# Kernel optimization log

Hardware: AMD Instinct MI355X
Metric: run time of the kernel (lower is better)

## Reference

```python
import jax, jax.numpy as jnp
import numpy as np

N = 50000      # total nodes across batch of graphs
E = 800000     # total directed edges (avg degree 16)
B = 64         # number of graphs
D = 128        # input_dim == hidden_dim
L = 4          # num_layers - 1 GIN layers
OUT = 10
BN_EPS = 1e-5


def setup_inputs() -> dict:
    key = jax.random.key(0)
    ks = jax.random.split(key, 12)
    s = 0.05
    return {
        "x": jax.random.normal(ks[0], (N, D), jnp.float32),
        "pi": jax.random.uniform(ks[1], (B, 25), jnp.float32),
        "eps": jnp.zeros((L,), jnp.float32),
        "mlp_w1": jax.random.normal(ks[2], (L, D, D), jnp.float32) * s,
        "mlp_b1": jnp.zeros((L, D), jnp.float32),
        "mlp_bn_g": jnp.ones((L, D), jnp.float32),
        "mlp_bn_b": jnp.zeros((L, D), jnp.float32),
        "mlp_w2": jax.random.normal(ks[3], (L, D, D), jnp.float32) * s,
        "mlp_b2": jnp.zeros((L, D), jnp.float32),
        "bn_g": jnp.ones((L, D), jnp.float32),
        "bn_b": jnp.zeros((L, D), jnp.float32),
        "attend_w": jax.random.normal(ks[4], (D * (L + 1), 1), jnp.float32) * s,
        "attend_b": jnp.zeros((1,), jnp.float32),
        "pi_w": jax.random.normal(ks[5], (25, 16), jnp.float32) * s,
        "pi_b": jnp.zeros((16,), jnp.float32),
        "out_w": jax.random.normal(ks[6], (D * (L + 1) + 16, OUT), jnp.float32) * s,
        "out_b": jnp.zeros((OUT,), jnp.float32),
        "edge_index": jax.random.randint(ks[7], (2, E), 0, N, dtype=jnp.int32),
        "graph_id": jnp.sort(jax.random.randint(ks[8], (N,), 0, B, dtype=jnp.int32)),
    }


def _bn(z, g, b):
    # BatchNorm1d in training mode over all nodes (axis 0)
    m = z.mean(axis=0)
    v = z.var(axis=0)
    return (z - m) * jax.lax.rsqrt(v + BN_EPS) * g + b


def reference(x, pi, eps, mlp_w1, mlp_b1, mlp_bn_g, mlp_bn_b, mlp_w2, mlp_b2,
              bn_g, bn_b, attend_w, attend_b, pi_w, pi_b, out_w, out_b,
              edge_index, graph_id):
    src, dst = edge_index[0], edge_index[1]
    h = x
    reps = [x]
    for l in range(L):
        # GIN sum aggregation (learn_eps=True: no self-loops in Adj)
        pooled = jax.ops.segment_sum(h[src], dst, num_segments=N)
        pooled = pooled + (1.0 + eps[l]) * h
        # 2-layer MLP: Linear -> BN -> ReLU -> Linear
        z = jax.nn.relu(_bn(pooled @ mlp_w1[l] + mlp_b1[l], mlp_bn_g[l], mlp_bn_b[l]))
        z = z @ mlp_w2[l] + mlp_b2[l]
        # outer BN + ReLU
        h = jax.nn.relu(_bn(z, bn_g[l], bn_b[l]))
        reps.append(h)
    hr = jnp.concatenate(reps, axis=1)               # [N, D*(L+1)]
    # per-graph attention softmax over nodes
    scores = (hr @ attend_w + attend_b)[:, 0]        # [N]
    smax = jax.ops.segment_max(scores, graph_id, num_segments=B)
    e = jnp.exp(scores - smax[graph_id])
    denom = jax.ops.segment_sum(e, graph_id, num_segments=B)
    coef = e / denom[graph_id]
    gemb = jax.ops.segment_sum(hr * coef[:, None], graph_id, num_segments=B)  # [B, D*(L+1)]
    # persistence-image branch (PI computed host-side; treated as input)
    pie = jax.nn.relu(pi @ pi_w + pi_b)              # [B, 16]
    feat = jnp.concatenate([gemb, pie], axis=1)      # [B, D*(L+1)+16]
    return feat @ out_w + out_b                      # [B, OUT]
```

## Files before the change

### kernel.cpp

```cpp
#include <hip/hip_runtime.h>
#include <hip/hip_bf16.h>

#define NN 50000
#define EE 800000
#define BBG 64
#define DD 128
#define LLAY 4
#define HRW 640
#define NOUT 10
#define SCANB 196
#define NXCD 8

typedef __hip_bfloat16 bf16;
typedef __attribute__((ext_vector_type(8))) short short8;
typedef __attribute__((ext_vector_type(4))) float f32x4;

__device__ __forceinline__ float b2f(bf16 v) { return __bfloat162float(v); }
__device__ __forceinline__ float bflo(unsigned u) { return __uint_as_float(u << 16); }
__device__ __forceinline__ float bfhi(unsigned u) { return __uint_as_float(u & 0xffff0000u); }
__device__ __forceinline__ unsigned short f2bs(float v) {
  bf16 h = __float2bfloat16(v);
  unsigned short r; __builtin_memcpy(&r, &h, 2); return r;
}
__device__ __forceinline__ int dtype_of(const void* __restrict__ bng) {
  return (*(const unsigned*)bng == 0x3F800000u) ? 1 : 0;
}
__device__ __forceinline__ float ldf(const void* __restrict__ p, long i, int dt) {
  return dt ? ((const float*)p)[i] : b2f(((const bf16*)p)[i]);
}

__device__ __forceinline__ int xccid() {
  unsigned v;
  asm("s_getreg_b32 %0, hwreg(HW_REG_XCC_ID)" : "=s"(v));
  return (int)(v & (NXCD - 1));
}

__device__ __forceinline__ void fadd_l2(float* p, float v) {
  asm volatile("global_atomic_add_f32 %0, %1, off" :: "v"(p), "v"(v) : "memory");
}

__device__ __forceinline__ int lower_bound_i(const int* __restrict__ a, int n, int key) {
  int lo = 0, hi = n;
  while (lo < hi) { int mid = (lo + hi) >> 1; if (a[mid] < key) lo = mid + 1; else hi = mid; }
  return lo;
}

__global__ __launch_bounds__(256) void gnn_init(const void* __restrict__ x,
                                                bf16* __restrict__ hrb,
                                                const void* __restrict__ w1,
                                                const void* __restrict__ w2,
                                                bf16* __restrict__ w1t,
                                                bf16* __restrict__ w2t,
                                                const void* __restrict__ aw,
                                                float* __restrict__ scores,
                                                const int* __restrict__ ei,
                                                int* __restrict__ cnt,
                                                int* __restrict__ rel,
                                                const void* __restrict__ bng) {
  int dt = dtype_of(bng);
  int tid = threadIdx.x;
  if (blockIdx.x >= 6250) {
    int i = (blockIdx.x - 6250) * 256 + tid;
    int l = i >> 14, rem = i & 16383, n = rem >> 7, k = rem & 127;
    long src = (long)l * 16384 + k * 128 + n;
    w1t[i] = __float2bfloat16(ldf(w1, src, dt));
    w2t[i] = __float2bfloat16(ldf(w2, src, dt));
    return;
  }
  if (blockIdx.x >= 3125) {
    int e = (blockIdx.x - 3125) * 256 + tid;
    int dst = ei[EE + e];
    int xid = xccid();
    int old = __hip_atomic_fetch_add(&cnt[(size_t)xid * NN + dst], 1,
                                     __ATOMIC_RELAXED, __HIP_MEMORY_SCOPE_WORKGROUP);
    rel[e] = (xid << 24) | old;
    return;
  }
  int n = blockIdx.x * 16 + (tid >> 4);
  int il = tid & 15;
  long base = (long)n * DD + il * 8;
  float v[8];
  if (dt) {
    float4 a0 = *(const float4*)((const float*)x + base);
    float4 a1 = *(const float4*)((const float*)x + base + 4);
    v[0] = a0.x; v[1] = a0.y; v[2] = a0.z; v[3] = a0.w;
    v[4] = a1.x; v[5] = a1.y; v[6] = a1.z; v[7] = a1.w;
  } else {
    uint4 u = *(const uint4*)((const bf16*)x + base);
    v[0] = bflo(u.x); v[1] = bfhi(u.x); v[2] = bflo(u.y); v[3] = bfhi(u.y);
    v[4] = bflo(u.z); v[5] = bfhi(u.z); v[6] = bflo(u.w); v[7] = bfhi(u.w);
  }
  uint4 o;
  o.x = (unsigned)f2bs(v[0]) | ((unsigned)f2bs(v[1]) << 16);
  o.y = (unsigned)f2bs(v[2]) | ((unsigned)f2bs(v[3]) << 16);
  o.z = (unsigned)f2bs(v[4]) | ((unsigned)f2bs(v[5]) << 16);
  o.w = (unsigned)f2bs(v[6]) | ((unsigned)f2bs(v[7]) << 16);
  *(uint4*)(hrb + (size_t)n * HRW + il * 8) = o;
  float ss = 0.f;
  #pragma unroll
  for (int k = 0; k < 8; k++) ss += v[k] * ldf(aw, il * 8 + k, dt);
  ss += __shfl_xor(ss, 1, 64); ss += __shfl_xor(ss, 2, 64);
  ss += __shfl_xor(ss, 4, 64); ss += __shfl_xor(ss, 8, 64);
  if (il == 0) scores[n] = ss;
}

__global__ __launch_bounds__(256) void gnn_scan1(const int* __restrict__ cnt,
                                                 int* __restrict__ blocksum) {
  __shared__ int buf[256];
  int tid = threadIdx.x;
  int i = blockIdx.x * 256 + tid;
  int v = 0;
  if (i < NN) {
    #pragma unroll
    for (int k = 0; k < NXCD; k++) v += cnt[(size_t)k * NN + i];
  }
  buf[tid] = v;
  __syncthreads();
  for (int s = 128; s > 0; s >>= 1) {
    if (tid < s) buf[tid] += buf[tid + s];
    __syncthreads();
  }
  if (tid == 0) blocksum[blockIdx.x] = buf[0];
}

__global__ __launch_bounds__(256) void gnn_scan3(int* __restrict__ cnt,
                                                 const int* __restrict__ blocksum,
                                                 int* __restrict__ rowstart) {
  __shared__ int buf[256];
  int tid = threadIdx.x;
  int partial = 0;
  for (int i = tid; i < blockIdx.x; i += 256) partial += blocksum[i];
  buf[tid] = partial;
  __syncthreads();
  for (int s = 128; s > 0; s >>= 1) {
    if (tid < s) buf[tid] += buf[tid + s];
    __syncthreads();
  }
  int offset = buf[0];
  __syncthreads();
  int i = blockIdx.x * 256 + tid;
  int c[NXCD];
  int v = 0;
  if (i < NN) {
    #pragma unroll
    for (int k = 0; k < NXCD; k++) { c[k] = cnt[(size_t)k * NN + i]; v += c[k]; }
  }
  buf[tid] = v;
  __syncthreads();
  for (int ofs = 1; ofs < 256; ofs <<= 1) {
    int t = (tid >= ofs) ? buf[tid - ofs] : 0;
    __syncthreads();
    buf[tid] += t;
    __syncthreads();
  }
  int val = offset + buf[tid] - v;
  if (i < NN) {
    rowstart[i] = val;
    int run = val;
    #pragma unroll
    for (int k = 0; k < NXCD; k++) { cnt[(size_t)k * NN + i] = run; run += c[k]; }
  }
  if (blockIdx.x == SCANB - 1 && tid == 255) rowstart[NN] = offset + buf[255];
}

__global__ __launch_bounds__(256) void gnn_fill(const int* __restrict__ ei,
                                                const int* __restrict__ xcdpre,
                                                const int* __restrict__ rel,
                                                int* __restrict__ csr_src) {
  int e = blockIdx.x * 256 + threadIdx.x;
  int src = ei[e];
  int dst = ei[EE + e];
  int r = rel[e];
  int xid = r >> 24;
  int rank = r & 0xFFFFFF;
  csr_src[xcdpre[(size_t)xid * NN + dst] + rank] = src;
}

__device__ __forceinline__ void acc8(float* a, uint4 u) {
  a[0] += bflo(u.x); a[1] += bfhi(u.x);
  a[2] += bflo(u.y); a[3] += bfhi(u.y);
  a[4] += bflo(u.z); a[5] += bfhi(u.z);
  a[6] += bflo(u.w); a[7] += bfhi(u.w);
}

__device__ __forceinline__ float2 statsum(const float* __restrict__ stat, int c) {
  float s = 0.f, q = 0.f;
  #pragma unroll
  for (int k = 0; k < 8; k++) { s += stat[k * 256 + c]; q += stat[k * 256 + 128 + c]; }
  return make_float2(s, q);
}

__global__ __launch_bounds__(512) void gnn_gmg1(const bf16* __restrict__ hrb, int l,
                                                const int* __restrict__ rowstart,
                                                const int* __restrict__ csr_src,
                                                const void* __restrict__ eps,
                                                const bf16* __restrict__ Wt,
                                                const void* __restrict__ bias, int biasOfs,
                                                bf16* __restrict__ out,
                                                float* __restrict__ statOut,
                                                const void* __restrict__ bng) {
  int dt = dtype_of(bng);
  __shared__ __align__(16) unsigned ar[16][68];
  __shared__ int qhead;
  int tid = threadIdx.x, lane = tid & 63;
  int w = tid >> 6;
  int q = lane >> 4, il = lane & 15;
  int r0 = blockIdx.x * 16;
  const bf16* stripe = hrb + l * DD;
  float s = 1.0f + ldf(eps, l, dt);
  if (tid == 0) qhead = 0;
  __syncthreads();

  for (;;) {
    int i;
    if (lane == 0) i = atomicAdd(&qhead, 1);
    i = __shfl(i, 0, 64);
    if (i >= 16) break;
    int n = r0 + i;
    float a[8] = {0.f, 0.f, 0.f, 0.f, 0.f, 0.f, 0.f, 0.f};
    if (q == 0) {
      uint4 u = *(const uint4*)(stripe + (size_t)n * HRW + il * 8);
      a[0] = s * bflo(u.x); a[1] = s * bfhi(u.x);
      a[2] = s * bflo(u.y); a[3] = s * bfhi(u.y);
      a[4] = s * bflo(u.z); a[5] = s * bfhi(u.z);
      a[6] = s * bflo(u.w); a[7] = s * bfhi(u.w);
    }
    int start = rowstart[n], end = rowstart[n + 1];
    for (int base = start; base < end; base += 64) {
      int m = end - base; if (m > 64) m = 64;
      int idx = (base + lane < end) ? csr_src[base + lane] : 0;
      int j = 0;
      for (; j + 16 <= m; j += 16) {
        int s0 = __shfl(idx, j + q, 64);
        int s1 = __shfl(idx, j + 4 + q, 64);
        int s2 = __shfl(idx, j + 8 + q, 64);
        int s3 = __shfl(idx, j + 12 + q, 64);
        uint4 u0 = *(const uint4*)(stripe + (size_t)s0 * HRW + il * 8);
        uint4 u1 = *(const uint4*)(stripe + (size_t)s1 * HRW + il * 8);
        uint4 u2 = *(const uint4*)(stripe + (size_t)s2 * HRW + il * 8);
        uint4 u3 = *(const uint4*)(stripe + (size_t)s3 * HRW + il * 8);
        acc8(a, u0); acc8(a, u1); acc8(a, u2); acc8(a, u3);
      }
      for (; j + 8 <= m; j += 8) {
        int s0 = __shfl(idx, j + q, 64);
        int s1 = __shfl(idx, j + 4 + q, 64);
        uint4 u0 = *(const uint4*)(stripe + (size_t)s0 * HRW + il * 8);
        uint4 u1 = *(const uint4*)(stripe + (size_t)s1 * HRW + il * 8);
        acc8(a, u0); acc8(a, u1);
      }
      for (; j + 4 <= m; j += 4) {
        int src = __shfl(idx, j + q, 64);
        uint4 u = *(const uint4*)(stripe + (size_t)src * HRW + il * 8);
        acc8(a, u);
      }
      for (; j < m; j++) {
        int src = __shfl(idx, j, 64);
        if (q == 0) {
          uint4 u = *(const uint4*)(stripe + (size_t)src * HRW + il * 8);
          acc8(a, u);
        }
      }
    }
    #pragma unroll
    for (int k = 0; k < 8; k++) {
      a[k] += __shfl_xor(a[k], 16, 64);
      a[k] += __shfl_xor(a[k], 32, 64);
    }
    if (q == 0) {
      uint4 o;
      o.x = (unsigned)f2bs(a[0]) | ((unsigned)f2bs(a[1]) << 16);
      o.y = (unsigned)f2bs(a[2]) | ((unsigned)f2bs(a[3]) << 16);
      o.z = (unsigned)f2bs(a[4]) | ((unsigned)f2bs(a[5]) << 16);
      o.w = (unsigned)f2bs(a[6]) | ((unsigned)f2bs(a[7]) << 16);
      *(uint4*)&ar[i][il * 4] = o;
    }
  }
  __syncthreads();

  f32x4 acc = (f32x4){0.f, 0.f, 0.f, 0.f};
  #pragma unroll
  for (int ch = 0; ch < 4; ch++) {
    int k0 = ch * 32 + q * 8;
    uint4 raw = *(const uint4*)&ar[il][ch * 16 + q * 4];
    short8 af;
    __builtin_memcpy(&af, &raw, 16);
    short8 bfv = *(const short8*)(Wt + (w * 16 + il) * DD + k0);
    acc = __builtin_amdgcn_mfma_f32_16x16x32_bf16(af, bfv, acc, 0, 0, 0);
  }
  int col = w * 16 + il;
  float bv = ldf(bias, biasOfs + col, dt);
  float ss = 0.f, qq = 0.f;
  #pragma unroll
  for (int r = 0; r < 4; r++) {
    int row = r0 + q * 4 + r;
    float v = acc[r] + bv;
    out[(size_t)row * DD + col] = __float2bfloat16(v);
    ss += v; qq += v * v;
  }
  ss += __shfl_xor(ss, 16, 64);  ss += __shfl_xor(ss, 32, 64);
  qq += __shfl_xor(qq, 16, 64);  qq += __shfl_xor(qq, 32, 64);
  if (q == 0) {
    int xid = xccid();
    fadd_l2(&statOut[xid * 256 + col], ss);
    fadd_l2(&statOut[xid * 256 + 128 + col], qq);
  }
}

__global__ __launch_bounds__(256) void gnn_mgemm(const bf16* __restrict__ Abf,
                                                 const bf16* __restrict__ Wt,
                                                 const void* __restrict__ bias, int biasOfs,
                                                 bf16* __restrict__ out,
                                                 const float* __restrict__ statIn,
                                                 const void* __restrict__ g,
                                                 const void* __restrict__ bb, int parOfs,
                                                 float* __restrict__ statOut,
                                                 const void* __restrict__ bng) {
  int dt = dtype_of(bng);
  __shared__ float scf[128], shf[128];
  __shared__ float redS[4][128], redQ[4][128];
  int tid = threadIdx.x, w = tid >> 6, lane = tid & 63;
  int q = lane >> 4, il = lane & 15;
  if (tid < 128) {
    const float invN = 1.0f / NN;
    float2 sq = statsum(statIn, tid);
    float m = sq.x * invN;
    float rs = rsqrtf(sq.y * invN - m * m + 1e-5f);
    float gg = ldf(g, parOfs + tid, dt), bv = ldf(bb, parOfs + tid, dt);
    scf[tid] = rs * gg;
    shf[tid] = bv - m * rs * gg;
  }
  __syncthreads();
  int r0 = (blockIdx.x * 4 + w) * 16;
  int arow = r0 + il;
  int arowc = (arow < NN) ? arow : (NN - 1);
  f32x4 acc[8];
  #pragma unroll
  for (int i = 0; i < 8; i++) acc[i] = (f32x4){0.f, 0.f, 0.f, 0.f};
  #pragma unroll
  for (int ch = 0; ch < 4; ch++) {
    int k0 = ch * 32 + q * 8;
    uint4 raw = *(const uint4*)(Abf + (size_t)arowc * DD + k0);
    float4 c0 = *(const float4*)(scf + k0);
    float4 c1 = *(const float4*)(scf + k0 + 4);
    float4 d0 = *(const float4*)(shf + k0);
    float4 d1 = *(const float4*)(shf + k0 + 4);
    short8 af;
    af[0] = (short)f2bs(fmaxf(bflo(raw.x) * c0.x + d0.x, 0.f));
    af[1] = (short)f2bs(fmaxf(bfhi(raw.x) * c0.y + d0.y, 0.f));
    af[2] = (short)f2bs(fmaxf(bflo(raw.y) * c0.z + d0.z, 0.f));
    af[3] = (short)f2bs(fmaxf(bfhi(raw.y) * c0.w + d0.w, 0.f));
    af[4] = (short)f2bs(fmaxf(bflo(raw.z) * c1.x + d1.x, 0.f));
    af[5] = (short)f2bs(fmaxf(bfhi(raw.z) * c1.y + d1.y, 0.f));
    af[6] = (short)f2bs(fmaxf(bflo(raw.w) * c1.z + d1.z, 0.f));
    af[7] = (short)f2bs(fmaxf(bfhi(raw.w) * c1.w + d1.w, 0.f));
    #pragma unroll
    for (int ct = 0; ct < 8; ct++) {
      short8 bfv = *(const short8*)(Wt + (ct * 16 + il) * DD + k0);
      acc[ct] = __builtin_amdgcn_mfma_f32_16x16x32_bf16(af, bfv, acc[ct], 0, 0, 0);
    }
  }
  #pragma unroll
  for (int ct = 0; ct < 8; ct++) {
    int col = ct * 16 + il;
    float bv = ldf(bias, biasOfs + col, dt);
    float s = 0.f, qq = 0.f;
    #pragma unroll
    for (int r = 0; r < 4; r++) {
      int row = r0 + q * 4 + r;
      float v = acc[ct][r] + bv;
      if (row < NN) {
        out[(size_t)row * DD + col] = __float2bfloat16(v);
        s += v; qq += v * v;
      }
    }
    s += __shfl_xor(s, 16, 64);  s += __shfl_xor(s, 32, 64);
    qq += __shfl_xor(qq, 16, 64); qq += __shfl_xor(qq, 32, 64);
    if (q == 0) { redS[w][col] = s; redQ[w][col] = qq; }
  }
  __syncthreads();
  int xid = xccid();
  if (tid < 128) {
    float v = redS[0][tid] + redS[1][tid] + redS[2][tid] + redS[3][tid];
    fadd_l2(&statOut[xid * 256 + tid], v);
  } else {
    int c = tid - 128;
    float v = redQ[0][c] + redQ[1][c] + redQ[2][c] + redQ[3][c];
    fadd_l2(&statOut[xid * 256 + 128 + c], v);
  }
}

__global__ __launch_bounds__(256) void gnn_bn_relu(const bf16* __restrict__ z2,
                                                   const float* __restrict__ stat,
                                                   const void* __restrict__ g,
                                                   const void* __restrict__ bb, int parOfs,
                                                   bf16* __restrict__ hrb, int stripe,
                                                   const void* __restrict__ aw,
                                                   float* __restrict__ scores,
                                                   const void* __restrict__ bng) {
  int dt = dtype_of(bng);
  __shared__ float scf[128], shf[128], awf[128];
  int tid = threadIdx.x;
  if (tid < 128) {
    const float invN = 1.0f / NN;
    float2 sq = statsum(stat, tid);
    float m = sq.x * invN;
    float rs = rsqrtf(sq.y * invN - m * m + 1e-5f);
    float gg = ldf(g, parOfs + tid, dt), bv = ldf(bb, parOfs + tid, dt);
    scf[tid] = rs * gg;
    shf[tid] = bv - m * rs * gg;
    awf[tid] = ldf(aw, stripe * DD + tid, dt);
  }
  __syncthreads();
  int n = blockIdx.x * 16 + (tid >> 4);
  int il = tid & 15;
  int c0 = il * 8;
  uint4 u = *(const uint4*)(z2 + (size_t)n * DD + c0);
  float v[8];
  v[0] = bflo(u.x); v[1] = bfhi(u.x); v[2] = bflo(u.y); v[3] = bfhi(u.y);
  v[4] = bflo(u.z); v[5] = bfhi(u.z); v[6] = bflo(u.w); v[7] = bfhi(u.w);
  float ss = 0.f;
  #pragma unroll
  for (int k = 0; k < 8; k++) {
    v[k] = fmaxf(v[k] * scf[c0 + k] + shf[c0 + k], 0.f);
    ss += v[k] * awf[c0 + k];
  }
  uint4 o;
  o.x = (unsigned)f2bs(v[0]) | ((unsigned)f2bs(v[1]) << 16);
  o.y = (unsigned)f2bs(v[2]) | ((unsigned)f2bs(v[3]) << 16);
  o.z = (unsigned)f2bs(v[4]) | ((unsigned)f2bs(v[5]) << 16);
  o.w = (unsigned)f2bs(v[6]) | ((unsigned)f2bs(v[7]) << 16);
  *(uint4*)(hrb + (size_t)n * HRW + stripe * DD + c0) = o;
  ss += __shfl_xor(ss, 1, 64); ss += __shfl_xor(ss, 2, 64);
  ss += __shfl_xor(ss, 4, 64); ss += __shfl_xor(ss, 8, 64);
  if (il == 0) scores[n] += ss;
}

__global__ __launch_bounds__(128) void gnn_gemb(const bf16* __restrict__ hrb,
                                                const float* __restrict__ scores,
                                                const int* __restrict__ gid,
                                                float* __restrict__ gemb) {
  int b = blockIdx.x / 40;
  int part = blockIdx.x % 40;
  int chunk = part % 5;
  int slice = part / 5;
  int tid = threadIdx.x;
  int start = lower_bound_i(gid, NN, b);
  int end = lower_bound_i(gid, NN, b + 1);
  __shared__ float red[128];
  float mx = -3.4e38f;
  for (int n = start + tid; n < end; n += 128) mx = fmaxf(mx, scores[n]);
  red[tid] = mx;
  __syncthreads();
  for (int s = 64; s > 0; s >>= 1) {
    if (tid < s) red[tid] = fmaxf(red[tid], red[tid + s]);
    __syncthreads();
  }
  float smax = red[0];
  __syncthreads();
  float sum = 0.f;
  for (int n = start + tid; n < end; n += 128) sum += __expf(scores[n] - smax);
  red[tid] = sum;
  __syncthreads();
  for (int s = 64; s > 0; s >>= 1) {
    if (tid < s) red[tid] += red[tid + s];
    __syncthreads();
  }
  float denom = red[0];
  float inv = (denom > 0.f) ? 1.0f / denom : 0.f;
  int c = chunk * 128 + tid;
  float acc = 0.f;
  for (int n = start + slice; n < end; n += 8)
    acc += b2f(hrb[(size_t)n * HRW + c]) * __expf(scores[n] - smax) * inv;
  unsafeAtomicAdd(&gemb[b * HRW + c], acc);
}

__global__ __launch_bounds__(64) void gnn_final(const float* __restrict__ gemb,
                                                const void* __restrict__ pi,
                                                const void* __restrict__ piw,
                                                const void* __restrict__ pib,
                                                const void* __restrict__ ow,
                                                const void* __restrict__ ob,
                                                void* __restrict__ out,
                                                const void* __restrict__ bng) {
  int dt = dtype_of(bng);
  int b = blockIdx.x;
  int t = threadIdx.x;
  __shared__ float pie[16];
  if (t < 16) {
    float s = ldf(pib, t, dt);
    for (int i = 0; i < 25; i++) s += ldf(pi, b * 25 + i, dt) * ldf(piw, i * 16 + t, dt);
    pie[t] = fmaxf(s, 0.f);
  }
  __syncthreads();
  for (int o = 0; o < NOUT; o++) {
    float s = 0.f;
    for (int c = t; c < HRW + 16; c += 64) {
      float f = (c < HRW) ? gemb[b * HRW + c] : pie[c - HRW];
      s += f * ldf(ow, c * NOUT + o, dt);
    }
    #pragma unroll
    for (int m = 32; m > 0; m >>= 1) s += __shfl_xor(s, m, 64);
    if (t == 0) {
      float r = s + ldf(ob, o, dt);
      if (dt) ((float*)out)[b * NOUT + o] = r;
      else ((bf16*)out)[b * NOUT + o] = __float2bfloat16(r);
    }
  }
}

extern "C" void kernel_launch(void* const* d_in, const int* in_sizes, int n_in,
                              void* d_out, int out_size, void* d_ws, size_t ws_size,
                              hipStream_t stream) {
  const void* x    = d_in[0];
  const void* pi   = d_in[1];
  const void* eps  = d_in[2];
  const void* w1   = d_in[3];
  const void* b1   = d_in[4];
  const void* bng  = d_in[5];
  const void* bnb  = d_in[6];
  const void* w2   = d_in[7];
  const void* b2   = d_in[8];
  const void* obng = d_in[9];
  const void* obnb = d_in[10];
  const void* aw   = d_in[11];
  const void* piw  = d_in[13];
  const void* pib  = d_in[14];
  const void* ow   = d_in[15];
  const void* ob   = d_in[16];
  const int*  ei   = (const int*)d_in[17];
  const int*  gid  = (const int*)d_in[18];

  bf16*  hrb      = (bf16*)d_ws;
  bf16*  z1       = hrb + (size_t)NN * HRW;
  bf16*  z2       = z1 + (size_t)NN * DD;
  bf16*  w1t      = z2 + (size_t)NN * DD;
  bf16*  w2t      = w1t + LLAY * DD * DD;
  float* statbufs = (float*)(w2t + LLAY * DD * DD);
  float* gemb     = statbufs + 8 * 2048;
  int*   cnt      = (int*)(gemb + BBG * HRW);
  size_t zeroBytes = (size_t)(8 * 2048 + BBG * HRW + NXCD * NN) * 4;
  float* scores   = (float*)(cnt + (size_t)NXCD * NN);
  int*   rowstart = (int*)(scores + NN);
  int*   rel      = rowstart + NN + 1;
  int*   csr_src  = rel + EE;
  int*   blocksum = csr_src + EE;

  hipMemsetAsync(statbufs, 0, zeroBytes, stream);
  gnn_init<<<6506, 256, 0, stream>>>(x, hrb, w1, w2, w1t, w2t, aw, scores,
                                     ei, cnt, rel, bng);

  gnn_scan1<<<SCANB, 256, 0, stream>>>(cnt, blocksum);
  gnn_scan3<<<SCANB, 256, 0, stream>>>(cnt, blocksum, rowstart);
  gnn_fill<<<EE / 256, 256, 0, stream>>>(ei, cnt, rel, csr_src);

  for (int l = 0; l < LLAY; l++) {
    float* statA = statbufs + (l * 2 + 0) * 2048;
    float* statB = statbufs + (l * 2 + 1) * 2048;
    gnn_gmg1<<<NN / 16, 512, 0, stream>>>(hrb, l, rowstart, csr_src, eps,
                                          w1t + l * DD * DD, b1, l * DD,
                                          z1, statA, bng);
    gnn_mgemm<<<782, 256, 0, stream>>>(z1, w2t + l * DD * DD, b2, l * DD,
                                       z2, statA, bng, bnb, l * DD,
                                       statB, bng);
    gnn_bn_relu<<<NN / 16, 256, 0, stream>>>(z2, statB, obng, obnb, l * DD,
                                             hrb, l + 1, aw, scores, bng);
  }

  gnn_gemb<<<BBG * 40, 128, 0, stream>>>(hrb, scores, gid, gemb);
  gnn_final<<<BBG, 64, 0, stream>>>(gemb, pi, piw, pib, ow, ob, d_out, bng);
}
```

Baseline: 556.4 us.

## Build CSR via two-level bucket sort and drop gemb atomics

Replaces the per-XCD atomic counting, two-kernel scan and scatter fill with a bucketed approach. Edges are binned by dst>>8 into 196 buckets using LDS atomics, then one block per bucket builds row offsets and the local CSR in shared memory. This cuts global atomics, kernel launches and the large zeroed count array. gemb now writes per-slice partials that gnn_final reduces instead of using float atomics. The risks are bucket overflow past BUCKCAP on skewed degree distributions and packing src into 16 bits, which truncates node ids above 65535.

After: 536.8 us. -3.5%, faster.

```diff
diff --git a/kernel.cpp b/kernel.cpp
--- a/kernel.cpp
+++ b/kernel.cpp
@@ -8,8 +8,11 @@
 #define LLAY 4
 #define HRW 640
 #define NOUT 10
-#define SCANB 196
 #define NXCD 8
+#define NBUCK 196
+#define BUCKCAP 4608
+#define EB 250
+#define ECH 3200
 
 typedef __hip_bfloat16 bf16;
 typedef __attribute__((ext_vector_type(8))) short short8;
@@ -54,13 +57,13 @@
                                                 const void* __restrict__ aw,
                                                 float* __restrict__ scores,
                                                 const int* __restrict__ ei,
-                                                int* __restrict__ cnt,
-                                                int* __restrict__ rel,
+                                                int* __restrict__ bucketCnt,
+                                                unsigned* __restrict__ bucketStore,
                                                 const void* __restrict__ bng) {
   int dt = dtype_of(bng);
   int tid = threadIdx.x;
-  if (blockIdx.x >= 6250) {
-    int i = (blockIdx.x - 6250) * 256 + tid;
+  if (blockIdx.x >= 3375) {
+    int i = (blockIdx.x - 3375) * 256 + tid;
     int l = i >> 14, rem = i & 16383, n = rem >> 7, k = rem & 127;
     long src = (long)l * 16384 + k * 128 + n;
     w1t[i] = __float2bfloat16(ldf(w1, src, dt));
@@ -68,12 +71,38 @@
     return;
   }
   if (blockIdx.x >= 3125) {
-    int e = (blockIdx.x - 3125) * 256 + tid;
-    int dst = ei[EE + e];
-    int xid = xccid();
-    int old = __hip_atomic_fetch_add(&cnt[(size_t)xid * NN + dst], 1,
-                                     __ATOMIC_RELAXED, __HIP_MEMORY_SCOPE_WORKGROUP);
-    rel[e] = (xid << 24) | old;
+    __shared__ int lcnt[NBUCK], gbase[NBUCK];
+    int bb = blockIdx.x - 3125;
+    int base = bb * ECH;
+    if (tid < NBUCK) lcnt[tid] = 0;
+    __syncthreads();
+    #pragma unroll
+    for (int j = 0; j < 13; j++) {
+      int k = j * 256 + tid;
+      if (k < ECH) {
+        int dst = ei[EE + base + k];
+        atomicAdd(&lcnt[dst >> 8], 1);
+      }
+    }
+    __syncthreads();
+    if (tid < NBUCK) {
+      gbase[tid] = atomicAdd(&bucketCnt[tid * 16], lcnt[tid]);
+      lcnt[tid] = 0;
+    }
+    __syncthreads();
+    #pragma unroll
+    for (int j = 0; j < 13; j++) {
+      int k = j * 256 + tid;
+      if (k < ECH) {
+        int e = base + k;
+        int src = ei[e];
+        int dst = ei[EE + e];
+        int b = dst >> 8;
+        int r = atomicAdd(&lcnt[b], 1);
+        bucketStore[b * BUCKCAP + gbase[b] + r] =
+            (unsigned)src | ((unsigned)(dst & 255) << 16);
+      }
+    }
     return;
   }
   int n = blockIdx.x * 16 + (tid >> 4);
@@ -104,48 +133,31 @@
   if (il == 0) scores[n] = ss;
 }
 
-__global__ __launch_bounds__(256) void gnn_scan1(const int* __restrict__ cnt,
-                                                 int* __restrict__ blocksum) {
-  __shared__ int buf[256];
-  int tid = threadIdx.x;
-  int i = blockIdx.x * 256 + tid;
-  int v = 0;
-  if (i < NN) {
-    #pragma unroll
-    for (int k = 0; k < NXCD; k++) v += cnt[(size_t)k * NN + i];
-  }
-  buf[tid] = v;
+__global__ __launch_bounds__(256) void gnn_csr(const int* __restrict__ bucketCnt,
+                                               const unsigned* __restrict__ bucketStore,
+                                               int* __restrict__ rowstart,
+                                               int* __restrict__ csr_src) {
+  __shared__ int cnt[256], dbase[256], buf[256];
+  int b = blockIdx.x, tid = threadIdx.x;
+  int p = (tid < b) ? bucketCnt[tid * 16] : 0;
+  buf[tid] = p;
   __syncthreads();
   for (int s = 128; s > 0; s >>= 1) {
     if (tid < s) buf[tid] += buf[tid + s];
     __syncthreads();
   }
-  if (tid == 0) blocksum[blockIdx.x] = buf[0];
-}
-
-__global__ __launch_bounds__(256) void gnn_scan3(int* __restrict__ cnt,
-                                                 const int* __restrict__ blocksum,
-                                                 int* __restrict__ rowstart) {
-  __shared__ int buf[256];
-  int tid = threadIdx.x;
-  int partial = 0;
-  for (int i = tid; i < blockIdx.x; i += 256) partial += blocksum[i];
-  buf[tid] = partial;
-  __syncthreads();
-  for (int s = 128; s > 0; s >>= 1) {
-    if (tid < s) buf[tid] += buf[tid + s];
-    __syncthreads();
-  }
-  int offset = buf[0];
-  __syncthreads();
-  int i = blockIdx.x * 256 + tid;
-  int c[NXCD];
-  int v = 0;
-  if (i < NN) {
-    #pragma unroll
-    for (int k = 0; k < NXCD; k++) { c[k] = cnt[(size_t)k * NN + i]; v += c[k]; }
-  }
-  buf[tid] = v;
+  int start = buf[0];
+  int sz = bucketCnt[b * 16];
+  __syncthreads();
+  cnt[tid] = 0;
+  __syncthreads();
+  for (int j = 0; j < 18; j++) {
+    int k = j * 256 + tid;
+    if (k < sz) atomicAdd(&cnt[bucketStore[b * BUCKCAP + k] >> 16], 1);
+  }
+  __syncthreads();
+  int c = cnt[tid];
+  buf[tid] = c;
   __syncthreads();
   for (int ofs = 1; ofs < 256; ofs <<= 1) {
     int t = (tid >= ofs) ? buf[tid - ofs] : 0;
@@ -153,27 +165,20 @@
     buf[tid] += t;
     __syncthreads();
   }
-  int val = offset + buf[tid] - v;
-  if (i < NN) {
-    rowstart[i] = val;
-    int run = val;
-    #pragma unroll
-    for (int k = 0; k < NXCD; k++) { cnt[(size_t)k * NN + i] = run; run += c[k]; }
-  }
-  if (blockIdx.x == SCANB - 1 && tid == 255) rowstart[NN] = offset + buf[255];
-}
-
-__global__ __launch_bounds__(256) void gnn_fill(const int* __restrict__ ei,
-                                                const int* __restrict__ xcdpre,
-                                                const int* __restrict__ rel,
-                                                int* __restrict__ csr_src) {
-  int e = blockIdx.x * 256 + threadIdx.x;
-  int src = ei[e];
-  int dst = ei[EE + e];
-  int r = rel[e];
-  int xid = r >> 24;
-  int rank = r & 0xFFFFFF;
-  csr_src[xcdpre[(size_t)xid * NN + dst] + rank] = src;
+  dbase[tid] = buf[tid] - c;
+  int d = b * 256 + tid;
+  if (d <= NN) rowstart[d] = start + buf[tid] - c;
+  cnt[tid] = 0;
+  __syncthreads();
+  for (int j = 0; j < 18; j++) {
+    int k = j * 256 + tid;
+    if (k < sz) {
+      unsigned v = bucketStore[b * BUCKCAP + k];
+      int dlo = v >> 16;
+      int r = atomicAdd(&cnt[dlo], 1);
+      csr_src[start + dbase[dlo] + r] = (int)(v & 0xFFFFu);
+    }
+  }
 }
 
 __device__ __forceinline__ void acc8(float* a, uint4 u) {
@@ -438,7 +443,7 @@
 __global__ __launch_bounds__(128) void gnn_gemb(const bf16* __restrict__ hrb,
                                                 const float* __restrict__ scores,
                                                 const int* __restrict__ gid,
-                                                float* __restrict__ gemb) {
+                                                float* __restrict__ gembp) {
   int b = blockIdx.x / 40;
   int part = blockIdx.x % 40;
   int chunk = part % 5;
@@ -471,10 +476,10 @@
   float acc = 0.f;
   for (int n = start + slice; n < end; n += 8)
     acc += b2f(hrb[(size_t)n * HRW + c]) * __expf(scores[n] - smax) * inv;
-  unsafeAtomicAdd(&gemb[b * HRW + c], acc);
-}
-
-__global__ __launch_bounds__(64) void gnn_final(const float* __restrict__ gemb,
+  gembp[((size_t)slice * BBG + b) * HRW + c] = acc;
+}
+
+__global__ __launch_bounds__(64) void gnn_final(const float* __restrict__ gembp,
                                                 const void* __restrict__ pi,
                                                 const void* __restrict__ piw,
                                                 const void* __restrict__ pib,
@@ -492,11 +497,25 @@
     pie[t] = fmaxf(s, 0.f);
   }
   __syncthreads();
+  float fv[11];
+  #pragma unroll
+  for (int i = 0; i < 11; i++) {
+    int c = t + i * 64;
+    float f = 0.f;
+    if (c < HRW) {
+      #pragma unroll
+      for (int s = 0; s < 8; s++) f += gembp[((size_t)s * BBG + b) * HRW + c];
+    } else if (c < HRW + 16) {
+      f = pie[c - HRW];
+    }
+    fv[i] = f;
+  }
   for (int o = 0; o < NOUT; o++) {
     float s = 0.f;
-    for (int c = t; c < HRW + 16; c += 64) {
-      float f = (c < HRW) ? gemb[b * HRW + c] : pie[c - HRW];
-      s += f * ldf(ow, c * NOUT + o, dt);
+    #pragma unroll
+    for (int i = 0; i < 11; i++) {
+      int c = t + i * 64;
+      if (c < HRW + 16) s += fv[i] * ldf(ow, (long)c * NOUT + o, dt);
     }
     #pragma unroll
     for (int m = 32; m > 0; m >>= 1) s += __shfl_xor(s, m, 64);
@@ -536,22 +555,18 @@
   bf16*  w1t      = z2 + (size_t)NN * DD;
   bf16*  w2t      = w1t + LLAY * DD * DD;
   float* statbufs = (float*)(w2t + LLAY * DD * DD);
-  float* gemb     = statbufs + 8 * 2048;
-  int*   cnt      = (int*)(gemb + BBG * HRW);
-  size_t zeroBytes = (size_t)(8 * 2048 + BBG * HRW + NXCD * NN) * 4;
-  float* scores   = (float*)(cnt + (size_t)NXCD * NN);
+  int*   bucketCnt= (int*)(statbufs + 8 * 2048);
+  size_t zeroBytes = (size_t)(8 * 2048 + NBUCK * 16) * 4;
+  float* gembp    = (float*)(bucketCnt + NBUCK * 16);
+  float* scores   = gembp + (size_t)8 * BBG * HRW;
   int*   rowstart = (int*)(scores + NN);
-  int*   rel      = rowstart + NN + 1;
-  int*   csr_src  = rel + EE;
-  int*   blocksum = csr_src + EE;
+  unsigned* bucketStore = (unsigned*)(rowstart + NN + 1);
+  int*   csr_src  = (int*)(bucketStore + (size_t)NBUCK * BUCKCAP);
 
   hipMemsetAsync(statbufs, 0, zeroBytes, stream);
-  gnn_init<<<6506, 256, 0, stream>>>(x, hrb, w1, w2, w1t, w2t, aw, scores,
-                                     ei, cnt, rel, bng);
-
-  gnn_scan1<<<SCANB, 256, 0, stream>>>(cnt, blocksum);
-  gnn_scan3<<<SCANB, 256, 0, stream>>>(cnt, blocksum, rowstart);
-  gnn_fill<<<EE / 256, 256, 0, stream>>>(ei, cnt, rel, csr_src);
+  gnn_init<<<3631, 256, 0, stream>>>(x, hrb, w1, w2, w1t, w2t, aw, scores,
+                                     ei, bucketCnt, bucketStore, bng);
+  gnn_csr<<<NBUCK, 256, 0, stream>>>(bucketCnt, bucketStore, rowstart, csr_src);
 
   for (int l = 0; l < LLAY; l++) {
     float* statA = statbufs + (l * 2 + 0) * 2048;
@@ -566,6 +581,6 @@
                                              hrb, l + 1, aw, scores, bng);
   }
 
-  gnn_gemb<<<BBG * 40, 128, 0, stream>>>(hrb, scores, gid, gemb);
-  gnn_final<<<BBG, 64, 0, stream>>>(gemb, pi, piw, pib, ow, ob, d_out, bng);
-}
+  gnn_gemb<<<BBG * 40, 128, 0, stream>>>(hrb, scores, gid, gembp);
+  gnn_final<<<BBG, 64, 0, stream>>>(gembp, pi, piw, pib, ow, ob, d_out, bng);
+}
```
